# Optimization experiments

Measured on AMD Instinct MI355X. Metric: run time of the kernel, lower is better.

Reference implementation:

```python
import jax, jax.numpy as jnp
import numpy as np

N, B, D, A, E, H = 8, 32768, 128, 64, 32, 128


def setup_inputs() -> dict:
    key = jax.random.key(0)
    ks = jax.random.split(key, 22)
    g = lambda k, shape: (jax.random.normal(k, shape, dtype=jnp.float32) * 0.1)
    return {
        "states": jax.random.normal(ks[0], (N, B, D), dtype=jnp.float32),
        # per-agent DQN (2-hidden-layer MLP), stacked over agents
        "W1": g(ks[1], (N, D, H)), "b1": g(ks[2], (N, H)),
        "W2": g(ks[3], (N, H, H)), "b2": g(ks[4], (N, H)),
        "W3": g(ks[5], (N, H, A)), "b3": g(ks[6], (N, A)),
        # per-agent query MLP
        "Wq1": g(ks[7], (N, D, E)), "bq1": g(ks[8], (N, E)),
        "Wq2": g(ks[9], (N, E, E)), "bq2": g(ks[10], (N, E)),
        # per-agent key Linear
        "Wk": g(ks[11], (N, D, E)), "bk": g(ks[12], (N, E)),
        # shared scaling MLP (D->1->1)
        "Ws1": g(ks[13], (D, 1)), "bs1": g(ks[14], (1,)),
        "Ws2": g(ks[15], (1, 1)), "bs2": g(ks[16], (1,)),
        # shared constraint MLP (D->E->1)
        "Wc1": g(ks[17], (D, E)), "bc1": g(ks[18], (E,)),
        "Wc2": g(ks[19], (E, 1)), "bc2": g(ks[20], (1,)),
    }


def reference(states, W1, b1, W2, b2, W3, b3, Wq1, bq1, Wq2, bq2, Wk, bk,
              Ws1, bs1, Ws2, bs2, Wc1, bc1, Wc2, bc2):
    relu = jax.nn.relu
    # per-agent DQN -> q_values [B, N, A]
    h = relu(jnp.einsum('nbd,ndh->nbh', states, W1) + b1[:, None, :])
    h = relu(jnp.einsum('nbh,nhk->nbk', h, W2) + b2[:, None, :])
    q_values = (jnp.einsum('nbh,nha->nba', h, W3) + b3[:, None, :]).transpose(1, 0, 2)
    # per-agent keys [B, N, E]
    keys = (jnp.einsum('nbd,nde->nbe', states, Wk) + bk[:, None, :]).transpose(1, 0, 2)
    # per-agent queries [B, N, E]
    qh = relu(jnp.einsum('nbd,nde->nbe', states, Wq1) + bq1[:, None, :])
    queries = (jnp.einsum('nbe,nef->nbf', qh, Wq2) + bq2[:, None, :]).transpose(1, 0, 2)
    # attention [B, N, N]
    scores = jnp.einsum('bnd,bmd->bnm', queries, keys) / jnp.sqrt(jnp.float32(E))
    attn = jax.nn.softmax(scores, axis=-1)
    # faithful to original einsum 'bnm,bna->bna' (sums attn over m)
    weighted_qs = jnp.einsum('bnm,bna->bna', attn, q_values)
    # shared scaling MLP, sigmoid gate [B, N, 1]
    s = relu(jnp.einsum('nbd,do->nbo', states, Ws1) + bs1)
    s = jnp.einsum('nbo,op->nbp', s, Ws2) + bs2
    scaling = jax.nn.sigmoid(s.transpose(1, 0, 2))
    summed_q = jnp.mean(scaling * weighted_qs, axis=1)  # [B, A]
    # shared constraint MLP [B, N, 1] -> mean over agents [B, 1]
    c = relu(jnp.einsum('nbd,de->nbe', states, Wc1) + bc1)
    c = (jnp.einsum('nbe,eo->nbo', c, Wc2) + bc2).transpose(1, 0, 2)
    c = jnp.mean(c, axis=1)
    return summed_q + c  # [B, A]
```

## Files before the change

### kernel.cpp

```cpp
#include <hip/hip_runtime.h>
#include <hip/hip_bf16.h>

#define NAG 8
#define BATCH 32768
#define DDIM 128
#define ADIM 64
#define HDIM 128

#define NJ1 11
#define NJ2 8
#define NJ3 4
#define FB_L1 (NJ1*4)
#define FB_L2 (NJ2*4)
#define FB_L3 (NJ3*4)
#define FB_B  (FB_L2+FB_L3)
#define FB_TOT (FB_L1+FB_L2+FB_L3)
#define WAGENT (FB_TOT*512)

typedef __attribute__((ext_vector_type(8))) short bf16x8;
typedef __attribute__((ext_vector_type(4))) float f32x4;
typedef __attribute__((ext_vector_type(4))) unsigned int u32x4;

static __device__ __forceinline__ unsigned short f2bf(float f) {
  unsigned int u = __builtin_bit_cast(unsigned int, f);
  u += 0x7fffu + ((u >> 16) & 1u);
  return (unsigned short)(u >> 16);
}

static __device__ __forceinline__ unsigned int cvt_pk_bf16(float a, float b) {
  unsigned int r;
  asm("v_cvt_pk_bf16_f32 %0, %1, %2" : "=v"(r) : "v"(a), "v"(b));
  return r;
}

static __device__ __forceinline__ void gload_lds16(const void* g, void* l) {
  __builtin_amdgcn_global_load_lds(
      (const __attribute__((address_space(1))) unsigned int*)g,
      (__attribute__((address_space(3))) unsigned int*)l, 16, 0, 0);
}

__global__ void __launch_bounds__(256)
prep_weights(const float* __restrict__ W1, const float* __restrict__ W2,
             const float* __restrict__ W3, const float* __restrict__ Wc1,
             const float* __restrict__ Ws1, const float* __restrict__ b1,
             const float* __restrict__ bc1, const float* __restrict__ bs1,
             unsigned short* __restrict__ wbuf, float* __restrict__ b1e)
{
  int tid = blockIdx.x * 256 + threadIdx.x;
  if (tid < NAG * WAGENT) {
    int agent = tid / WAGENT;
    int rem   = tid % WAGENT;
    int fb = rem >> 9;
    int li = rem & 511;
    int l = li >> 3, t = li & 7;
    int lr = l & 15, lg = l >> 4;
    float v = 0.0f;
    if (fb < FB_L1) {
      int j = fb >> 2, kk = fb & 3;
      int col = j*16 + lr, k = kk*32 + lg*8 + t;
      if (col < 128)       v = W1[((size_t)agent*128 + k)*128 + col];
      else if (col < 160)  v = Wc1[k*32 + (col-128)];
      else if (col == 160) v = Ws1[k];
    } else if (fb < FB_L1 + FB_L2) {
      int f = fb - FB_L1;
      int j = f >> 2, kk = f & 3;
      int col = j*16 + lr, k = kk*32 + lg*8 + t;
      v = W2[((size_t)agent*128 + k)*128 + col];
    } else {
      int f = fb - FB_L1 - FB_L2;
      int j = f >> 2, kk = f & 3;
      int col = j*16 + lr, k = kk*32 + lg*8 + t;
      v = W3[((size_t)agent*128 + k)*64 + col];
    }
    wbuf[tid] = f2bf(v);
  }
  if (tid < NAG * 176) {
    int agent = tid / 176, col = tid % 176;
    float v = 0.0f;
    if (col < 128)       v = b1[agent*128 + col];
    else if (col < 160)  v = bc1[col - 128];
    else if (col == 160) v = bs1[0];
    b1e[tid] = v;
  }
}

__global__ void __launch_bounds__(512, 1)
qatten_main(const float* __restrict__ states,
            const float* __restrict__ b2g, const float* __restrict__ b3g,
            const float* __restrict__ ws2p, const float* __restrict__ bs2p,
            const float* __restrict__ wc2g, const float* __restrict__ bc2p,
            const unsigned short* __restrict__ wbuf,
            const float* __restrict__ b1e,
            float* __restrict__ out)
{
  __shared__ __align__(16) unsigned short bufA[FB_L1*512];
  __shared__ __align__(16) unsigned short bufB[FB_B*512];
  __shared__ __align__(16) unsigned short hlds[8 * 4096];

  const int tid  = threadIdx.x;
  const int wave = tid >> 6;
  const int lane = tid & 63;
  const int lr   = lane & 15;
  const int lg   = lane >> 4;
  const int row0 = blockIdx.x * 256 + wave * 32;
  const int abase = blockIdx.y * 4;

  unsigned short* hp = hlds + wave * 4096;

  const float ws2  = ws2p[0];
  const float bs2v = bs2p[0];
  const float bc2v = bc2p[0];
  const float wc2a = wc2g[lr];
  const float wc2b = wc2g[16 + lr];

  const f32x4 zero4 = {0.f, 0.f, 0.f, 0.f};

  f32x4 out_acc[2][NJ3];
#pragma unroll
  for (int m = 0; m < 2; ++m)
#pragma unroll
    for (int j = 0; j < NJ3; ++j) out_acc[m][j] = zero4;

  {
    const char* sA = (const char*)(wbuf + (size_t)abase * WAGENT);
    for (int c = wave; c < FB_L1; c += 8)
      gload_lds16(sA + c*1024 + lane*16, (char*)bufA + c*1024);
    const char* sB = sA + FB_L1*1024;
    for (int c = wave; c < FB_B; c += 8)
      gload_lds16(sB + c*1024 + lane*16, (char*)bufB + c*1024);
  }
  __syncthreads();

  for (int a4 = 0; a4 < 4; ++a4) {
    const int a = abase + a4;

    bf16x8 afr[2][4];
    {
      const float* sb = states + ((size_t)a * BATCH + row0) * DDIM;
#pragma unroll
      for (int m = 0; m < 2; ++m)
#pragma unroll
        for (int kk = 0; kk < 4; ++kk) {
          const float* p = sb + (m*16 + lr)*DDIM + kk*32 + lg*8;
          f32x4 v0 = *(const f32x4*)p;
          f32x4 v1 = *(const f32x4*)(p + 4);
          u32x4 w;
          w[0] = cvt_pk_bf16(v0[0], v0[1]);
          w[1] = cvt_pk_bf16(v0[2], v0[3]);
          w[2] = cvt_pk_bf16(v1[0], v1[1]);
          w[3] = cvt_pk_bf16(v1[2], v1[3]);
          afr[m][kk] = __builtin_bit_cast(bf16x8, w);
        }
    }

    float b1v[NJ1];
#pragma unroll
    for (int j = 0; j < NJ1; ++j) b1v[j] = b1e[a*176 + j*16 + lr];

    f32x4 eacc[3][2];
    {
      bf16x8 pf[2][4];
#pragma unroll
      for (int kk = 0; kk < 4; ++kk)
        pf[0][kk] = *(const bf16x8*)&bufA[kk*512 + lane*8];
#pragma unroll
      for (int j = 0; j < 11; ++j) {
        if (j < 10) {
#pragma unroll
          for (int kk = 0; kk < 4; ++kk)
            pf[(j+1)&1][kk] = *(const bf16x8*)&bufA[((j+1)*4 + kk)*512 + lane*8];
        }
#pragma unroll
        for (int m = 0; m < 2; ++m) {
          f32x4 acc = zero4;
#pragma unroll
          for (int kk = 0; kk < 4; ++kk)
            acc = __builtin_amdgcn_mfma_f32_16x16x32_bf16(afr[m][kk], pf[j&1][kk], acc, 0, 0, 0);
          if (j < 8) {
#pragma unroll
            for (int r = 0; r < 4; ++r) {
              float hv = acc[r] + b1v[j];
              hv = hv > 0.f ? hv : 0.f;
              int row = m*16 + lg*4 + r;
              int bo = row*256 + (((j*16 + lr)*2) ^ ((row & 7) << 4));
              *(unsigned short*)((char*)hp + bo) = f2bf(hv);
            }
          } else {
            eacc[j-8][m] = acc;
          }
        }
      }
    }

    float scl[2][4], crow[2][4];
#pragma unroll
    for (int m = 0; m < 2; ++m)
#pragma unroll
      for (int r = 0; r < 4; ++r) {
        float c0 = eacc[0][m][r] + b1v[8];  c0 = c0 > 0.f ? c0 : 0.f;
        float c1 = eacc[1][m][r] + b1v[9];  c1 = c1 > 0.f ? c1 : 0.f;
        float cd = c0*wc2a + c1*wc2b;
        cd += __shfl_xor(cd, 1);
        cd += __shfl_xor(cd, 2);
        cd += __shfl_xor(cd, 4);
        cd += __shfl_xor(cd, 8);
        crow[m][r] = cd + bc2v;
        float sp = eacc[2][m][r] + b1v[10];
        sp = __shfl(sp, lane & 48);
        sp = sp > 0.f ? sp : 0.f;
        float s = ws2 * sp + bs2v;
        scl[m][r] = 1.f / (1.f + __expf(-s));
      }

#pragma unroll
    for (int m = 0; m < 2; ++m)
#pragma unroll
      for (int kk = 0; kk < 4; ++kk) {
        int row = m*16 + lr;
        int bo = row*256 + ((kk*64 + lg*16) ^ ((row & 7) << 4));
        afr[m][kk] = *(const bf16x8*)((char*)hp + bo);
      }

    __syncthreads();

    if (a4 < 3) {
      const char* sA = (const char*)(wbuf + (size_t)(a+1)*WAGENT);
      for (int c = wave; c < FB_L1; c += 8)
        gload_lds16(sA + c*1024 + lane*16, (char*)bufA + c*1024);
    }

    {
      float b2v[NJ2];
#pragma unroll
      for (int j = 0; j < NJ2; ++j) b2v[j] = b2g[a*HDIM + j*16 + lr];
      bf16x8 pf[2][4];
#pragma unroll
      for (int kk = 0; kk < 4; ++kk)
        pf[0][kk] = *(const bf16x8*)&bufB[kk*512 + lane*8];
#pragma unroll
      for (int j = 0; j < 8; ++j) {
        if (j < 7) {
#pragma unroll
          for (int kk = 0; kk < 4; ++kk)
            pf[(j+1)&1][kk] = *(const bf16x8*)&bufB[((j+1)*4 + kk)*512 + lane*8];
        }
#pragma unroll
        for (int m = 0; m < 2; ++m) {
          f32x4 acc = zero4;
#pragma unroll
          for (int kk = 0; kk < 4; ++kk)
            acc = __builtin_amdgcn_mfma_f32_16x16x32_bf16(afr[m][kk], pf[j&1][kk], acc, 0, 0, 0);
#pragma unroll
          for (int r = 0; r < 4; ++r) {
            float hv = acc[r] + b2v[j];
            hv = hv > 0.f ? hv : 0.f;
            int row = m*16 + lg*4 + r;
            int bo = row*256 + (((j*16 + lr)*2) ^ ((row & 7) << 4));
            *(unsigned short*)((char*)hp + bo) = f2bf(hv);
          }
        }
      }
    }

#pragma unroll
    for (int m = 0; m < 2; ++m)
#pragma unroll
      for (int kk = 0; kk < 4; ++kk) {
        int row = m*16 + lr;
        int bo = row*256 + ((kk*64 + lg*16) ^ ((row & 7) << 4));
        afr[m][kk] = *(const bf16x8*)((char*)hp + bo);
      }

    {
      float b3v[NJ3];
#pragma unroll
      for (int j = 0; j < NJ3; ++j) b3v[j] = b3g[a*ADIM + j*16 + lr];
      bf16x8 pf[2][4];
#pragma unroll
      for (int kk = 0; kk < 4; ++kk)
        pf[0][kk] = *(const bf16x8*)&bufB[(FB_L2 + kk)*512 + lane*8];
#pragma unroll
      for (int j = 0; j < NJ3; ++j) {
        if (j < NJ3-1) {
#pragma unroll
          for (int kk = 0; kk < 4; ++kk)
            pf[(j+1)&1][kk] = *(const bf16x8*)&bufB[(FB_L2 + (j+1)*4 + kk)*512 + lane*8];
        }
#pragma unroll
        for (int m = 0; m < 2; ++m) {
          f32x4 acc = zero4;
#pragma unroll
          for (int kk = 0; kk < 4; ++kk)
            acc = __builtin_amdgcn_mfma_f32_16x16x32_bf16(afr[m][kk], pf[j&1][kk], acc, 0, 0, 0);
#pragma unroll
          for (int r = 0; r < 4; ++r)
            out_acc[m][j][r] += scl[m][r] * (acc[r] + b3v[j]) + crow[m][r];
        }
      }
    }

    __syncthreads();

    if (a4 < 3) {
      const char* sB = (const char*)(wbuf + (size_t)(a+1)*WAGENT + FB_L1*512);
      for (int c = wave; c < FB_B; c += 8)
        gload_lds16(sB + c*1024 + lane*16, (char*)bufB + c*1024);
    }
  }

#pragma unroll
  for (int m = 0; m < 2; ++m)
#pragma unroll
    for (int j = 0; j < NJ3; ++j)
#pragma unroll
      for (int r = 0; r < 4; ++r) {
        size_t row = (size_t)row0 + m*16 + lg*4 + r;
        atomicAdd(&out[row*ADIM + j*16 + lr], out_acc[m][j][r] * 0.125f);
      }
}

extern "C" void kernel_launch(void* const* d_in, const int* in_sizes, int n_in,
                              void* d_out, int out_size, void* d_ws, size_t ws_size,
                              hipStream_t stream)
{
  const float* states = (const float*)d_in[0];
  const float* W1  = (const float*)d_in[1];
  const float* b1  = (const float*)d_in[2];
  const float* W2  = (const float*)d_in[3];
  const float* b2  = (const float*)d_in[4];
  const float* W3  = (const float*)d_in[5];
  const float* b3  = (const float*)d_in[6];
  const float* Ws1 = (const float*)d_in[13];
  const float* bs1 = (const float*)d_in[14];
  const float* Ws2 = (const float*)d_in[15];
  const float* bs2 = (const float*)d_in[16];
  const float* Wc1 = (const float*)d_in[17];
  const float* bc1 = (const float*)d_in[18];
  const float* Wc2 = (const float*)d_in[19];
  const float* bc2 = (const float*)d_in[20];

  unsigned short* wbuf = (unsigned short*)d_ws;
  float* b1e = (float*)((char*)d_ws + (size_t)NAG * WAGENT * 2);

  hipMemsetAsync(d_out, 0, (size_t)out_size * sizeof(float), stream);

  dim3 pb(256), pg((NAG * WAGENT + 255) / 256);
  prep_weights<<<pg, pb, 0, stream>>>(W1, W2, W3, Wc1, Ws1, b1, bc1, bs1, wbuf, b1e);

  dim3 mb(512), mg(BATCH / 256, 2);
  qatten_main<<<mg, mb, 0, stream>>>(states, b2, b3, Ws2, bs2, Wc2, bc2,
                                     wbuf, b1e, (float*)d_out);
}
```

Baseline: 73.87 us.

## Shrink blocks to 256 threads with a single shared weight buffer for occupancy

Halves the block size to 4 waves and 128 rows, and merges the separate layer-1 and layer-2/3 weight LDS buffers into one buffer that is reloaded synchronously before each phase. The aim is to cut LDS use per block so several blocks can share a CU, and to drop the launch_bounds min-block constraint. In exchange the prefetch overlap is lost: each weight load now sits behind a barrier, and each block loads the weights twice as often in total. It also switches the scalar bf16 conversion to the hardware pack instruction.

```diff
diff --git a/kernel.cpp b/kernel.cpp
--- a/kernel.cpp
+++ b/kernel.cpp
@@ -31,6 +31,12 @@
   unsigned int r;
   asm("v_cvt_pk_bf16_f32 %0, %1, %2" : "=v"(r) : "v"(a), "v"(b));
   return r;
+}
+
+static __device__ __forceinline__ unsigned short f2bf1(float f) {
+  unsigned int r;
+  asm("v_cvt_pk_bf16_f32 %0, %1, %2" : "=v"(r) : "v"(f), "v"(f));
+  return (unsigned short)r;
 }
 
 static __device__ __forceinline__ void gload_lds16(const void* g, void* l) {
@@ -84,7 +90,7 @@
   }
 }
 
-__global__ void __launch_bounds__(512, 1)
+__global__ void __launch_bounds__(256)
 qatten_main(const float* __restrict__ states,
             const float* __restrict__ b2g, const float* __restrict__ b3g,
             const float* __restrict__ ws2p, const float* __restrict__ bs2p,
@@ -93,16 +99,15 @@
             const float* __restrict__ b1e,
             float* __restrict__ out)
 {
-  __shared__ __align__(16) unsigned short bufA[FB_L1*512];
-  __shared__ __align__(16) unsigned short bufB[FB_B*512];
-  __shared__ __align__(16) unsigned short hlds[8 * 4096];
+  __shared__ __align__(16) unsigned short bufW[FB_B*512];
+  __shared__ __align__(16) unsigned short hlds[4 * 4096];
 
   const int tid  = threadIdx.x;
   const int wave = tid >> 6;
   const int lane = tid & 63;
   const int lr   = lane & 15;
   const int lg   = lane >> 4;
-  const int row0 = blockIdx.x * 256 + wave * 32;
+  const int row0 = blockIdx.x * 128 + wave * 32;
   const int abase = blockIdx.y * 4;
 
   unsigned short* hp = hlds + wave * 4096;
@@ -123,16 +128,17 @@
 
   {
     const char* sA = (const char*)(wbuf + (size_t)abase * WAGENT);
-    for (int c = wave; c < FB_L1; c += 8)
-      gload_lds16(sA + c*1024 + lane*16, (char*)bufA + c*1024);
-    const char* sB = sA + FB_L1*1024;
-    for (int c = wave; c < FB_B; c += 8)
-      gload_lds16(sB + c*1024 + lane*16, (char*)bufB + c*1024);
+    for (int c = wave; c < FB_L1; c += 4)
+      gload_lds16(sA + c*1024 + lane*16, (char*)bufW + c*1024);
   }
   __syncthreads();
 
   for (int a4 = 0; a4 < 4; ++a4) {
     const int a = abase + a4;
+
+    float b1v[NJ1];
+#pragma unroll
+    for (int j = 0; j < NJ1; ++j) b1v[j] = b1e[a*176 + j*16 + lr];
 
     bf16x8 afr[2][4];
     {
@@ -153,22 +159,18 @@
         }
     }
 
-    float b1v[NJ1];
-#pragma unroll
-    for (int j = 0; j < NJ1; ++j) b1v[j] = b1e[a*176 + j*16 + lr];
-
     f32x4 eacc[3][2];
     {
       bf16x8 pf[2][4];
 #pragma unroll
       for (int kk = 0; kk < 4; ++kk)
-        pf[0][kk] = *(const bf16x8*)&bufA[kk*512 + lane*8];
+        pf[0][kk] = *(const bf16x8*)&bufW[kk*512 + lane*8];
 #pragma unroll
       for (int j = 0; j < 11; ++j) {
         if (j < 10) {
 #pragma unroll
           for (int kk = 0; kk < 4; ++kk)
-            pf[(j+1)&1][kk] = *(const bf16x8*)&bufA[((j+1)*4 + kk)*512 + lane*8];
+            pf[(j+1)&1][kk] = *(const bf16x8*)&bufW[((j+1)*4 + kk)*512 + lane*8];
         }
 #pragma unroll
         for (int m = 0; m < 2; ++m) {
@@ -183,7 +185,7 @@
               hv = hv > 0.f ? hv : 0.f;
               int row = m*16 + lg*4 + r;
               int bo = row*256 + (((j*16 + lr)*2) ^ ((row & 7) << 4));
-              *(unsigned short*)((char*)hp + bo) = f2bf(hv);
+              *(unsigned short*)((char*)hp + bo) = f2bf1(hv);
             }
           } else {
             eacc[j-8][m] = acc;
@@ -223,11 +225,13 @@
 
     __syncthreads();
 
-    if (a4 < 3) {
-      const char* sA = (const char*)(wbuf + (size_t)(a+1)*WAGENT);
-      for (int c = wave; c < FB_L1; c += 8)
-        gload_lds16(sA + c*1024 + lane*16, (char*)bufA + c*1024);
-    }
+    {
+      const char* sB = (const char*)(wbuf + (size_t)a*WAGENT + FB_L1*512);
+      for (int c = wave; c < FB_B; c += 4)
+        gload_lds16(sB + c*1024 + lane*16, (char*)bufW + c*1024);
+    }
+
+    __syncthreads();
 
     {
       float b2v[NJ2];
@@ -236,13 +240,13 @@
       bf16x8 pf[2][4];
 #pragma unroll
       for (int kk = 0; kk < 4; ++kk)
-        pf[0][kk] = *(const bf16x8*)&bufB[kk*512 + lane*8];
+        pf[0][kk] = *(const bf16x8*)&bufW[kk*512 + lane*8];
 #pragma unroll
       for (int j = 0; j < 8; ++j) {
         if (j < 7) {
 #pragma unroll
           for (int kk = 0; kk < 4; ++kk)
-            pf[(j+1)&1][kk] = *(const bf16x8*)&bufB[((j+1)*4 + kk)*512 + lane*8];
+            pf[(j+1)&1][kk] = *(const bf16x8*)&bufW[((j+1)*4 + kk)*512 + lane*8];
         }
 #pragma unroll
         for (int m = 0; m < 2; ++m) {
@@ -256,7 +260,7 @@
             hv = hv > 0.f ? hv : 0.f;
             int row = m*16 + lg*4 + r;
             int bo = row*256 + (((j*16 + lr)*2) ^ ((row & 7) << 4));
-            *(unsigned short*)((char*)hp + bo) = f2bf(hv);
+            *(unsigned short*)((char*)hp + bo) = f2bf1(hv);
           }
         }
       }
@@ -278,13 +282,13 @@
       bf16x8 pf[2][4];
 #pragma unroll
       for (int kk = 0; kk < 4; ++kk)
-        pf[0][kk] = *(const bf16x8*)&bufB[(FB_L2 + kk)*512 + lane*8];
+        pf[0][kk] = *(const bf16x8*)&bufW[(FB_L2 + kk)*512 + lane*8];
 #pragma unroll
       for (int j = 0; j < NJ3; ++j) {
         if (j < NJ3-1) {
 #pragma unroll
           for (int kk = 0; kk < 4; ++kk)
-            pf[(j+1)&1][kk] = *(const bf16x8*)&bufB[(FB_L2 + (j+1)*4 + kk)*512 + lane*8];
+            pf[(j+1)&1][kk] = *(const bf16x8*)&bufW[(FB_L2 + (j+1)*4 + kk)*512 + lane*8];
         }
 #pragma unroll
         for (int m = 0; m < 2; ++m) {
@@ -302,10 +306,12 @@
     __syncthreads();
 
     if (a4 < 3) {
-      const char* sB = (const char*)(wbuf + (size_t)(a+1)*WAGENT + FB_L1*512);
-      for (int c = wave; c < FB_B; c += 8)
-        gload_lds16(sB + c*1024 + lane*16, (char*)bufB + c*1024);
-    }
+      const char* sA = (const char*)(wbuf + (size_t)(a+1)*WAGENT);
+      for (int c = wave; c < FB_L1; c += 4)
+        gload_lds16(sA + c*1024 + lane*16, (char*)bufW + c*1024);
+    }
+
+    __syncthreads();
   }
 
 #pragma unroll
@@ -347,7 +353,7 @@
   dim3 pb(256), pg((NAG * WAGENT + 255) / 256);
   prep_weights<<<pg, pb, 0, stream>>>(W1, W2, W3, Wc1, Ws1, b1, bc1, bs1, wbuf, b1e);
 
-  dim3 mb(512), mg(BATCH / 256, 2);
+  dim3 mb(256), mg(BATCH / 128, 2);
   qatten_main<<<mg, mb, 0, stream>>>(states, b2, b3, Ws2, bs2, Wc2, bc2,
                                      wbuf, b1e, (float*)d_out);
 }
```

Measured after the change: 88.82 us. 20.2% more time.
